# Optimization experiments

Hardware: AMD Instinct MI355X
Metric: run time of the kernel (lower is better)

Reference implementation:

```python
import jax, jax.numpy as jnp
import numpy as np

H = 768
NH = 12
HD = H // NH
NDIM = 5
LN_EPS = 1e-5


def setup_inputs() -> dict:
    key = jax.random.key(0)
    ks = jax.random.split(key, 12)
    B, S = 4, 2048
    xavier = lambda k: jax.random.uniform(k, (H, H), jnp.float32, -1.0, 1.0) * np.sqrt(6.0 / (H + H))
    return {
        "hidden_states": jax.random.normal(ks[0], (B, S, H), jnp.float32),
        "Wq": xavier(ks[1]), "bq": jnp.zeros((H,), jnp.float32),
        "Wk": xavier(ks[2]), "bk": jnp.zeros((H,), jnp.float32),
        "Wv": xavier(ks[3]), "bv": jnp.zeros((H,), jnp.float32),
        "Wo": xavier(ks[4]), "bo": jnp.zeros((H,), jnp.float32),
        # per-dimension, per-head scalar biases (torch init: zeros; use small randn so grads are non-trivial)
        "dim_biases": 0.02 * jax.random.normal(ks[5], (NDIM, NH), jnp.float32),
        "ln_gamma": jnp.ones((H,), jnp.float32),
        "ln_beta": jnp.zeros((H,), jnp.float32),
        "attention_mask": jax.random.randint(ks[6], (4, 2048), 0, 2, jnp.int32),
        "dimension_idx": 2,
    }


def reference(hidden_states, Wq, bq, Wk, bk, Wv, bv, Wo, bo, dim_biases,
              ln_gamma, ln_beta, attention_mask, dimension_idx):
    B, S, _ = hidden_states.shape
    residual = hidden_states
    # torch nn.Linear: x @ W.T + b
    q = (hidden_states @ Wq.T + bq).reshape(B, S, NH, HD).transpose(0, 2, 1, 3)  # [B,NH,S,HD]
    k = (hidden_states @ Wk.T + bk).reshape(B, S, NH, HD).transpose(0, 2, 1, 3)
    v = (hidden_states @ Wv.T + bv).reshape(B, S, NH, HD).transpose(0, 2, 1, 3)

    scores = jnp.einsum("bhqd,bhkd->bhqk", q, k) / np.sqrt(HD)  # [B,NH,S,S]
    if dimension_idx is not None and dimension_idx < NDIM:
        scores = scores + dim_biases[dimension_idx][None, :, None, None]
    # mask over key positions, broadcast over heads and queries
    scores = jnp.where(attention_mask[:, None, None, :] == 0, -jnp.inf, scores)
    attn = jax.nn.softmax(scores, axis=-1)

    ctx = jnp.einsum("bhqk,bhkd->bhqd", attn, v)  # [B,NH,S,HD]
    ctx = ctx.transpose(0, 2, 1, 3).reshape(B, S, H)
    out = ctx @ Wo.T + bo

    y = out + residual
    mu = jnp.mean(y, axis=-1, keepdims=True)
    var = jnp.var(y, axis=-1, keepdims=True)
    y = (y - mu) / jnp.sqrt(var + LN_EPS) * ln_gamma + ln_beta
    return y
```

## Files before the change

### kernel.cpp

```cpp
#include <hip/hip_runtime.h>
#include <hip/hip_bf16.h>

#define HH    768
#define NHEAD 12
#define HDIM  64
#define BB    4
#define SS    2048
#define MM    (BB*SS)
#define NDIMS 5
#define WEL   (HH*HH)
#define LOG2E 1.44269504088896f
#define QSCALE 0.180336881f

typedef unsigned short u16;
typedef __attribute__((ext_vector_type(8))) short short8;
typedef __attribute__((ext_vector_type(4))) short short4v;
typedef __attribute__((ext_vector_type(4))) float floatx4;
typedef __attribute__((ext_vector_type(16))) float floatx16;
typedef __attribute__((ext_vector_type(4))) unsigned int uint4v;
typedef __attribute__((ext_vector_type(2))) unsigned int uint2v;

__device__ __forceinline__ float bf2f(u16 u) {
    return __uint_as_float(((unsigned int)u) << 16);
}
__device__ __forceinline__ u16 f2bf(float f) {
    unsigned int x = __float_as_uint(f);
    unsigned int r = (x + 0x7fffu + ((x >> 16) & 1u)) >> 16;
    return (u16)r;
}
__device__ __forceinline__ unsigned int pack_bf16x2(float a, float b) {
    float2 f2 = make_float2(a, b);
    __hip_bfloat162 h2 = __float22bfloat162_rn(f2);
    return *reinterpret_cast<unsigned int*>(&h2);
}
__device__ __forceinline__ void gld16(const u16* g, u16* l) {
    __builtin_amdgcn_global_load_lds(
        (const __attribute__((address_space(1))) unsigned int*)g,
        (__attribute__((address_space(3))) unsigned int*)l, 16, 0, 0);
}

__global__ __launch_bounds__(256) void f32_to_bf16(
    const float* __restrict__ in, u16* __restrict__ out, int n8)
{
    int i = blockIdx.x * 256 + threadIdx.x;
    if (i >= n8) return;
    float4 a = ((const float4*)in)[i*2];
    float4 b = ((const float4*)in)[i*2 + 1];
    ushort4 lo, hi;
    lo.x = f2bf(a.x); lo.y = f2bf(a.y); lo.z = f2bf(a.z); lo.w = f2bf(a.w);
    hi.x = f2bf(b.x); hi.y = f2bf(b.y); hi.z = f2bf(b.z); hi.w = f2bf(b.w);
    ((ushort4*)out)[i*2]     = lo;
    ((ushort4*)out)[i*2 + 1] = hi;
}

#define XCVT_BLKS ((MM*HH)/8/256)
#define WCVT_BLKS (WEL/8/256)
__global__ __launch_bounds__(256) void cvt_all(
    const float* __restrict__ x,
    const float* __restrict__ W0, const float* __restrict__ W1,
    const float* __restrict__ W2, const float* __restrict__ W3,
    u16* __restrict__ xb, u16* __restrict__ wb)
{
    const int bid = blockIdx.x;
    const float* src;
    u16* dst;
    int i;
    if (bid < XCVT_BLKS) {
        src = x; dst = xb; i = bid * 256 + threadIdx.x;
    } else {
        const int wsel = (bid - XCVT_BLKS) / WCVT_BLKS;
        src = (wsel == 0) ? W0 : (wsel == 1) ? W1 : (wsel == 2) ? W2 : W3;
        dst = wb + (size_t)wsel * WEL;
        i = ((bid - XCVT_BLKS) % WCVT_BLKS) * 256 + threadIdx.x;
    }
    float4 a = ((const float4*)src)[i*2];
    float4 b = ((const float4*)src)[i*2 + 1];
    ushort4 lo, hi;
    lo.x = f2bf(a.x); lo.y = f2bf(a.y); lo.z = f2bf(a.z); lo.w = f2bf(a.w);
    hi.x = f2bf(b.x); hi.y = f2bf(b.y); hi.z = f2bf(b.z); hi.w = f2bf(b.w);
    ((ushort4*)dst)[i*2]     = lo;
    ((ushort4*)dst)[i*2 + 1] = hi;
}

__device__ __forceinline__ void gemm_gld_body(
    const u16* __restrict__ Xb, const u16* __restrict__ Wrows,
    const float* __restrict__ biasL, u16* __restrict__ outL, int i0)
{
    __shared__ u16 Xs[128][64];
    __shared__ u16 Ws[128][64];
    const int t = threadIdx.x;
    const int w = t >> 6, lane = t & 63;
    const int wy = w >> 1, wx = w & 1;
    const int m = lane & 31, hh = lane >> 5;

    const int grow = lane >> 3;
    const int cg   = (lane & 7) ^ grow;

    floatx16 acc[2][2];
    #pragma unroll
    for (int am = 0; am < 2; ++am)
        #pragma unroll
        for (int bn = 0; bn < 2; ++bn)
            #pragma unroll
            for (int r = 0; r < 16; ++r) acc[am][bn][r] = 0.f;

    for (int k0 = 0; k0 < HH; k0 += 64) {
        __syncthreads();
        #pragma unroll
        for (int j = 0; j < 4; ++j) {
            const int r = w*32 + j*8;
            gld16(Xb    + (size_t)(i0 + r + grow)*HH + k0 + cg*8, &Xs[r][0]);
            gld16(Wrows + (size_t)(r + grow)*HH      + k0 + cg*8, &Ws[r][0]);
        }
        __syncthreads();

        #pragma unroll
        for (int kh = 0; kh < 4; ++kh) {
            const int ch = kh*2 + hh;
            short8 af[2], bf[2];
            #pragma unroll
            for (int am = 0; am < 2; ++am) {
                const int row = wy*64 + am*32 + m;
                af[am] = *(const short8*)&Xs[row][(ch ^ (m & 7))*8];
            }
            #pragma unroll
            for (int bn = 0; bn < 2; ++bn) {
                const int row = wx*64 + bn*32 + m;
                bf[bn] = *(const short8*)&Ws[row][(ch ^ (m & 7))*8];
            }
            #pragma unroll
            for (int am = 0; am < 2; ++am)
                #pragma unroll
                for (int bn = 0; bn < 2; ++bn)
                    acc[am][bn] = __builtin_amdgcn_mfma_f32_32x32x16_bf16(
                        af[am], bf[bn], acc[am][bn], 0, 0, 0);
        }
    }

    float bb[2];
    #pragma unroll
    for (int bn = 0; bn < 2; ++bn) bb[bn] = biasL[wx*64 + bn*32 + m];
    #pragma unroll
    for (int am = 0; am < 2; ++am)
        #pragma unroll
        for (int bn = 0; bn < 2; ++bn)
            #pragma unroll
            for (int r = 0; r < 16; ++r) {
                int row = i0 + wy*64 + am*32 + (r & 3) + 8*(r >> 2) + 4*hh;
                outL[(size_t)row*HH + wx*64 + bn*32 + m] = f2bf(acc[am][bn][r] + bb[bn]);
            }
}

__global__ __launch_bounds__(256) void gemm_gld_qkv(
    const u16* __restrict__ Xb, const u16* __restrict__ Wb3,
    const float* __restrict__ bq, const float* __restrict__ bk, const float* __restrict__ bv,
    u16* __restrict__ oq, u16* __restrict__ ok, u16* __restrict__ ov)
{
    const int j0 = blockIdx.x * 128;
    const int sel = j0 / HH;
    const int lj = j0 - sel * HH;
    const float* bias = (sel == 0) ? bq : (sel == 1) ? bk : bv;
    u16* out = (sel == 0) ? oq : (sel == 1) ? ok : ov;
    gemm_gld_body(Xb, Wb3 + (size_t)j0 * HH, bias + lj, out + lj, blockIdx.y * 128);
}

__global__ __launch_bounds__(256) void gemm_gld_single(
    const u16* __restrict__ Xb, const u16* __restrict__ Wb,
    const float* __restrict__ bias, u16* __restrict__ out)
{
    const int j0 = blockIdx.x * 128;
    gemm_gld_body(Xb, Wb + (size_t)j0 * HH, bias + j0, out + j0, blockIdx.y * 128);
}

__global__ __launch_bounds__(256) void gemm_mfma_nt(
    const u16* __restrict__ Xb, const float* __restrict__ W,
    const float* __restrict__ bias, u16* __restrict__ out)
{
    __shared__ u16 Xs[128][40];
    __shared__ u16 Wt[64][40];
    const int t = threadIdx.x;
    const int w = t >> 6, lane = t & 63;
    const int c = lane & 15, qd = lane >> 4;
    const int i0 = blockIdx.y * 128, j0 = blockIdx.x * 64;
    const int xrow = t >> 1, xoff = (t & 1) * 16;
    const int wn = t >> 2, woff = (t & 3) * 8;

    floatx4 acc[2][4];
    #pragma unroll
    for (int mt = 0; mt < 2; ++mt)
        #pragma unroll
        for (int nt = 0; nt < 4; ++nt) acc[mt][nt] = (floatx4){0.f,0.f,0.f,0.f};

    for (int k0 = 0; k0 < HH; k0 += 32) {
        uint4 xa  = *(const uint4*)(Xb + (size_t)(i0 + xrow)*HH + k0 + xoff);
        uint4 xb2 = *(const uint4*)(Xb + (size_t)(i0 + xrow)*HH + k0 + xoff + 8);
        float4 wa = *(const float4*)(W + (size_t)(j0 + wn)*HH + k0 + woff);
        float4 wb = *(const float4*)(W + (size_t)(j0 + wn)*HH + k0 + woff + 4);
        __syncthreads();
        *(uint4*)&Xs[xrow][xoff]     = xa;
        *(uint4*)&Xs[xrow][xoff + 8] = xb2;
        ushort4 w0, w1;
        w0.x = f2bf(wa.x); w0.y = f2bf(wa.y); w0.z = f2bf(wa.z); w0.w = f2bf(wa.w);
        w1.x = f2bf(wb.x); w1.y = f2bf(wb.y); w1.z = f2bf(wb.z); w1.w = f2bf(wb.w);
        *(ushort4*)&Wt[wn][woff]     = w0;
        *(ushort4*)&Wt[wn][woff + 4] = w1;
        __syncthreads();

        short8 a0 = *(const short8*)&Xs[w*32 + c][qd*8];
        short8 a1 = *(const short8*)&Xs[w*32 + 16 + c][qd*8];
        #pragma unroll
        for (int nt = 0; nt < 4; ++nt) {
            short8 bfr = *(const short8*)&Wt[nt*16 + c][qd*8];
            acc[0][nt] = __builtin_amdgcn_mfma_f32_16x16x32_bf16(a0, bfr, acc[0][nt], 0, 0, 0);
            acc[1][nt] = __builtin_amdgcn_mfma_f32_16x16x32_bf16(a1, bfr, acc[1][nt], 0, 0, 0);
        }
    }

    float bv[4];
    #pragma unroll
    for (int nt = 0; nt < 4; ++nt) bv[nt] = bias[j0 + nt*16 + c];
    #pragma unroll
    for (int mt = 0; mt < 2; ++mt)
        #pragma unroll
        for (int nt = 0; nt < 4; ++nt)
            #pragma unroll
            for (int r = 0; r < 4; ++r)
                out[(size_t)(i0 + w*32 + mt*16 + qd*4 + r)*HH + j0 + nt*16 + c] =
                    f2bf(acc[mt][nt][r] + bv[nt]);
}

__global__ __launch_bounds__(256, 3) void attn_mfma32(
    const u16* __restrict__ Q, const u16* __restrict__ K, const u16* __restrict__ V,
    const float* __restrict__ dim_biases, const int* __restrict__ mask,
    const int* __restrict__ dim_idx_p, u16* __restrict__ ctx)
{
    __shared__ u16 Ks[2][64][64];
    __shared__ u16 Vt[2][64][68];
    __shared__ float madd[2][64];

    const int t = threadIdx.x;
    const int w = t >> 6, lane = t & 63;
    const int ql = lane & 31, hi = lane >> 5;
    const int sw7 = ql & 7;

    const int flat = blockIdx.x + 16 * (blockIdx.y + 12 * blockIdx.z);
    const int swz  = (flat & 7) * 96 + (flat >> 3);
    const int q0 = (swz & 15) * 128;
    const int h  = (swz >> 4) % NHEAD;
    const int b  = swz / (16 * NHEAD);

    const int didx = *dim_idx_p;
    const float db2 = ((didx < NDIMS) ? dim_biases[didx*NHEAD + h] : 0.f) * LOG2E;

    const int grow = lane >> 3;
    const int cg   = (lane & 7) ^ grow;
    const int vkp = t & 31;
    const int vdg = (t >> 5) * 8;

    short8 ones;
    #pragma unroll
    for (int j = 0; j < 8; ++j) ones[j] = (short)0x3F80;

    short8 qv[4];
    {
        const u16* qsrc = Q + ((size_t)(b*SS + q0 + w*32 + ql))*HH + h*HDIM + 8*hi;
        #pragma unroll
        for (int s = 0; s < 4; ++s) {
            ushort4 u0 = *(const ushort4*)(qsrc + s*16);
            ushort4 u1 = *(const ushort4*)(qsrc + s*16 + 4);
            const u16 uu[8] = {u0.x,u0.y,u0.z,u0.w,u1.x,u1.y,u1.z,u1.w};
            #pragma unroll
            for (int j = 0; j < 8; ++j)
                qv[s][j] = (short)f2bf(bf2f(uu[j]) * QSCALE);
        }
    }

    floatx16 o[2], lacc;
    #pragma unroll
    for (int r = 0; r < 16; ++r) { o[0][r] = 0.f; o[1][r] = 0.f; lacc[r] = 0.f; }

    uint4 VA, VB;
    int mreg = 0;

    auto issueK = [&](int kt, int buf) {
        #pragma unroll
        for (int j = 0; j < 2; ++j) {
            const int rbase = w*16 + j*8;
            gld16(K + (size_t)(b*SS + kt*64 + rbase + grow)*HH + h*HDIM + cg*8,
                  &Ks[buf][rbase][0]);
        }
    };
    auto issueV = [&](int kt) {
        const u16* va = V + ((size_t)(b*SS + kt*64 + 2*vkp))*HH + h*HDIM + vdg;
        VA = *(const uint4*)va;
        VB = *(const uint4*)(va + HH);
        if (t < 64) mreg = mask[(size_t)b*SS + kt*64 + t];
    };
    auto writeV = [&](int buf) {
        const unsigned* Aw = (const unsigned*)&VA;
        const unsigned* Bw = (const unsigned*)&VB;
        #pragma unroll
        for (int i2 = 0; i2 < 4; ++i2) {
            unsigned a = Aw[i2], bb = Bw[i2];
            *(unsigned*)&Vt[buf][vdg + 2*i2][2*vkp]     = (a & 0xffffu) | (bb << 16);
            *(unsigned*)&Vt[buf][vdg + 2*i2 + 1][2*vkp] = (a >> 16) | (bb & 0xffff0000u);
        }
        if (t < 64) madd[buf][t] = (mreg != 0) ? db2 : -1e30f;
    };

    issueK(0, 0);
    issueV(0);
    writeV(0);

    for (int kt = 0; kt < SS/64; ++kt) {
        const int cur = kt & 1;
        __syncthreads();
        const bool more = (kt + 1 < SS/64);
        if (more) { issueK(kt + 1, cur ^ 1); issueV(kt + 1); }

        #pragma unroll
        for (int kblk = 0; kblk < 2; ++kblk) {
            const u16* kb = &Ks[cur][kblk*32 + ql][0];

            floatx16 z;
            #pragma unroll
            for (int qq = 0; qq < 4; ++qq) {
                float4 mv = *(const float4*)&madd[cur][kblk*32 + qq*8 + 4*hi];
                z[qq*4+0] = mv.x; z[qq*4+1] = mv.y; z[qq*4+2] = mv.z; z[qq*4+3] = mv.w;
            }
            short8 kf[4];
            #pragma unroll
            for (int s = 0; s < 4; ++s)
                kf[s] = *(const short8*)(kb + ((s*2 + hi) ^ sw7)*8);
            __builtin_amdgcn_s_setprio(1);
            #pragma unroll
            for (int s = 0; s < 4; ++s)
                z = __builtin_amdgcn_mfma_f32_32x32x16_bf16(kf[s], qv[s], z, 0, 0, 0);
            __builtin_amdgcn_s_setprio(0);

            #pragma unroll
            for (int r = 0; r < 16; ++r) z[r] = __builtin_amdgcn_exp2f(z[r]);

            #pragma unroll
            for (int ks = 0; ks < 2; ++ks) {
                unsigned x0 = pack_bf16x2(z[ks*8 + 0], z[ks*8 + 1]);
                unsigned y0 = pack_bf16x2(z[ks*8 + 4], z[ks*8 + 5]);
                unsigned x1 = pack_bf16x2(z[ks*8 + 2], z[ks*8 + 3]);
                unsigned y1 = pack_bf16x2(z[ks*8 + 6], z[ks*8 + 7]);
                uint2v s0 = __builtin_amdgcn_permlane32_swap(x0, y0, false, false);
                uint2v s1 = __builtin_amdgcn_permlane32_swap(x1, y1, false, false);
                uint4v pv; pv[0] = s0[0]; pv[1] = s1[0]; pv[2] = s0[1]; pv[3] = s1[1];
                short8 pa = __builtin_bit_cast(short8, pv);

                const int ck = kblk*4 + ks*2 + hi;
                const u16* vp0 = &Vt[cur][ql][ck*8];
                const u16* vp1 = &Vt[cur][32 + ql][ck*8];
                short4v a0 = *(const short4v*)vp0;
                short4v a1 = *(const short4v*)(vp0 + 4);
                short4v b0 = *(const short4v*)vp1;
                short4v b1 = *(const short4v*)(vp1 + 4);
                short8 vf0, vf1;
                #pragma unroll
                for (int j = 0; j < 4; ++j) {
                    vf0[j] = a0[j]; vf0[4+j] = a1[j];
                    vf1[j] = b0[j]; vf1[4+j] = b1[j];
                }

                __builtin_amdgcn_s_setprio(1);
                lacc = __builtin_amdgcn_mfma_f32_32x32x16_bf16(pa, ones, lacc, 0, 0, 0);
                o[0] = __builtin_amdgcn_mfma_f32_32x32x16_bf16(pa, vf0, o[0], 0, 0, 0);
                o[1] = __builtin_amdgcn_mfma_f32_32x32x16_bf16(pa, vf1, o[1], 0, 0, 0);
                __builtin_amdgcn_s_setprio(0);
            }
        }

        if (more) writeV(cur ^ 1);
    }

    #pragma unroll
    for (int r = 0; r < 16; ++r) {
        float l = lacc[r];
        float inv = (l > 0.f) ? 1.f / l : 0.f;
        const int qrow = q0 + w*32 + (r & 3) + 8*(r >> 2) + 4*hi;
        u16* dst = ctx + ((size_t)(b*SS + qrow))*HH + h*HDIM + ql;
        dst[0]  = f2bf(o[0][r] * inv);
        dst[32] = f2bf(o[1][r] * inv);
    }
}

__global__ __launch_bounds__(256) void add_ln_wave(
    const u16* __restrict__ proj, const float* __restrict__ resid,
    const float* __restrict__ gamma, const float* __restrict__ beta,
    float* __restrict__ out)
{
    const int t = threadIdx.x, w = t >> 6, lane = t & 63;
    const int row = blockIdx.x * 4 + w;
    const size_t base = (size_t)row * HH + lane * 12;
    const int gbase = lane * 12;

    float x[12];
    #pragma unroll
    for (int j = 0; j < 3; ++j) {
        ushort4 p = *(const ushort4*)(proj + base + j*4);
        float4  r = *(const float4*)(resid + base + j*4);
        x[j*4+0] = bf2f(p.x) + r.x;
        x[j*4+1] = bf2f(p.y) + r.y;
        x[j*4+2] = bf2f(p.z) + r.z;
        x[j*4+3] = bf2f(p.w) + r.w;
    }
    float s = 0.f, ss = 0.f;
    #pragma unroll
    for (int j = 0; j < 12; ++j) { s += x[j]; ss += x[j]*x[j]; }
    #pragma unroll
    for (int off = 1; off < 64; off <<= 1) {
        s  += __shfl_xor(s, off);
        ss += __shfl_xor(ss, off);
    }
    float mean = s * (1.f/768.f);
    float var  = ss * (1.f/768.f) - mean*mean;
    float rstd = rsqrtf(fmaxf(var, 0.f) + 1e-5f);
    #pragma unroll
    for (int j = 0; j < 3; ++j) {
        float4 g = *(const float4*)(gamma + gbase + j*4);
        float4 bt = *(const float4*)(beta + gbase + j*4);
        float4 y;
        y.x = (x[j*4+0]-mean)*rstd*g.x + bt.x;
        y.y = (x[j*4+1]-mean)*rstd*g.y + bt.y;
        y.z = (x[j*4+2]-mean)*rstd*g.z + bt.z;
        y.w = (x[j*4+3]-mean)*rstd*g.w + bt.w;
        *(float4*)(out + base + j*4) = y;
    }
}

extern "C" void kernel_launch(void* const* d_in, const int* in_sizes, int n_in,
                              void* d_out, int out_size, void* d_ws, size_t ws_size,
                              hipStream_t stream)
{
    (void)in_sizes; (void)n_in; (void)out_size;
    const float* x    = (const float*)d_in[0];
    const float* Wq   = (const float*)d_in[1];
    const float* bq   = (const float*)d_in[2];
    const float* Wk   = (const float*)d_in[3];
    const float* bk   = (const float*)d_in[4];
    const float* Wv   = (const float*)d_in[5];
    const float* bv   = (const float*)d_in[6];
    const float* Wo   = (const float*)d_in[7];
    const float* bo   = (const float*)d_in[8];
    const float* dimb = (const float*)d_in[9];
    const float* gam  = (const float*)d_in[10];
    const float* bet  = (const float*)d_in[11];
    const int* mask   = (const int*)d_in[12];
    const int* didx   = (const int*)d_in[13];

    const size_t N = (size_t)MM * HH;
    if (ws_size < 4 * N * sizeof(u16)) return;
    u16* ws = (u16*)d_ws;
    u16* q    = ws;
    u16* kbuf = ws + N;
    u16* vbuf = ws + 2*N;
    u16* slot3 = ws + 3*N;
    u16* xb   = slot3;
    u16* ctx  = slot3;
    u16* proj = q;

    const bool bigws = ws_size >= (4 * N + 4 * (size_t)WEL) * sizeof(u16);
    u16* wb = ws + 4 * N;

    if (bigws) {
        cvt_all<<<XCVT_BLKS + 4*WCVT_BLKS, 256, 0, stream>>>(x, Wq, Wk, Wv, Wo, xb, wb);
        gemm_gld_qkv<<<dim3(3*HH/128, MM/128), 256, 0, stream>>>(
            xb, wb, bq, bk, bv, q, kbuf, vbuf);
    } else {
        f32_to_bf16<<<(int)(N/8/256), 256, 0, stream>>>(x, xb, (int)(N/8));
        dim3 gg(HH/64, MM/128);
        gemm_mfma_nt<<<gg, 256, 0, stream>>>(xb, Wq, bq, q);
        gemm_mfma_nt<<<gg, 256, 0, stream>>>(xb, Wk, bk, kbuf);
        gemm_mfma_nt<<<gg, 256, 0, stream>>>(xb, Wv, bv, vbuf);
    }
    attn_mfma32<<<dim3(SS/128, NHEAD, BB), 256, 0, stream>>>(q, kbuf, vbuf, dimb, mask, didx, ctx);
    if (bigws) gemm_gld_single<<<dim3(HH/128, MM/128), 256, 0, stream>>>(ctx, wb + 3*WEL, bo, proj);
    else {
        dim3 gg(HH/64, MM/128);
        gemm_mfma_nt<<<gg, 256, 0, stream>>>(ctx, Wo, bo, proj);
    }
    add_ln_wave<<<MM/4, 256, 0, stream>>>(proj, x, gam, bet, (float*)d_out);
}
```

Before: 245.6 us.

## Swizzle QKV GEMM block order and add 64-row tile kernel for output projection

The QKV GEMM now remaps its flat block index so that groups of 8 consecutive blocks are spread across the grid, aiming for better L2/cache locality or XCD distribution. The output projection switches from 128x128 tiles to a new 64x128 tile kernel with the same swizzled block mapping, doubling the block count to 768 for better CU occupancy on the 256-CU part. Smaller tiles reduce data reuse per block and add a new kernel body to maintain.

```diff
diff --git a/kernel.cpp b/kernel.cpp
--- a/kernel.cpp
+++ b/kernel.cpp
@@ -156,20 +156,74 @@
     const float* __restrict__ bq, const float* __restrict__ bk, const float* __restrict__ bv,
     u16* __restrict__ oq, u16* __restrict__ ok, u16* __restrict__ ov)
 {
-    const int j0 = blockIdx.x * 128;
+    const int flat = blockIdx.x + 18 * blockIdx.y;
+    const int swz  = (flat & 7) * 144 + (flat >> 3);
+    const int j0 = (swz % 18) * 128;
+    const int i0 = (swz / 18) * 128;
     const int sel = j0 / HH;
     const int lj = j0 - sel * HH;
     const float* bias = (sel == 0) ? bq : (sel == 1) ? bk : bv;
     u16* out = (sel == 0) ? oq : (sel == 1) ? ok : ov;
-    gemm_gld_body(Xb, Wb3 + (size_t)j0 * HH, bias + lj, out + lj, blockIdx.y * 128);
-}
-
-__global__ __launch_bounds__(256) void gemm_gld_single(
+    gemm_gld_body(Xb, Wb3 + (size_t)j0 * HH, bias + lj, out + lj, i0);
+}
+
+__global__ __launch_bounds__(256) void gemm_gld_m64(
     const u16* __restrict__ Xb, const u16* __restrict__ Wb,
     const float* __restrict__ bias, u16* __restrict__ out)
 {
-    const int j0 = blockIdx.x * 128;
-    gemm_gld_body(Xb, Wb + (size_t)j0 * HH, bias + j0, out + j0, blockIdx.y * 128);
+    __shared__ u16 Xs[64][64];
+    __shared__ u16 Ws[128][64];
+    const int t = threadIdx.x;
+    const int w = t >> 6, lane = t & 63;
+    const int m = lane & 31, hh = lane >> 5;
+    const int grow = lane >> 3;
+    const int cg   = (lane & 7) ^ grow;
+
+    const int flat = blockIdx.x + 6 * blockIdx.y;
+    const int swz  = (flat & 7) * 96 + (flat >> 3);
+    const int j0 = (swz % 6) * 128;
+    const int i0 = (swz / 6) * 64;
+
+    floatx16 acc[2];
+    #pragma unroll
+    for (int am = 0; am < 2; ++am)
+        #pragma unroll
+        for (int r = 0; r < 16; ++r) acc[am][r] = 0.f;
+
+    for (int k0 = 0; k0 < HH; k0 += 64) {
+        __syncthreads();
+        #pragma unroll
+        for (int j = 0; j < 2; ++j) {
+            const int r = w*16 + j*8;
+            gld16(Xb + (size_t)(i0 + r + grow)*HH + k0 + cg*8, &Xs[r][0]);
+        }
+        #pragma unroll
+        for (int j = 0; j < 4; ++j) {
+            const int r = w*32 + j*8;
+            gld16(Wb + (size_t)(j0 + r + grow)*HH + k0 + cg*8, &Ws[r][0]);
+        }
+        __syncthreads();
+
+        #pragma unroll
+        for (int kh = 0; kh < 4; ++kh) {
+            const int ch = kh*2 + hh;
+            short8 af[2], bf;
+            af[0] = *(const short8*)&Xs[m][(ch ^ (m & 7))*8];
+            af[1] = *(const short8*)&Xs[32 + m][(ch ^ (m & 7))*8];
+            bf    = *(const short8*)&Ws[w*32 + m][(ch ^ (m & 7))*8];
+            acc[0] = __builtin_amdgcn_mfma_f32_32x32x16_bf16(af[0], bf, acc[0], 0, 0, 0);
+            acc[1] = __builtin_amdgcn_mfma_f32_32x32x16_bf16(af[1], bf, acc[1], 0, 0, 0);
+        }
+    }
+
+    const float bb = bias[j0 + w*32 + m];
+    #pragma unroll
+    for (int am = 0; am < 2; ++am)
+        #pragma unroll
+        for (int r = 0; r < 16; ++r) {
+            int row = i0 + am*32 + (r & 3) + 8*(r >> 2) + 4*hh;
+            out[(size_t)row*HH + j0 + w*32 + m] = f2bf(acc[am][r] + bb);
+        }
 }
 
 __global__ __launch_bounds__(256) void gemm_mfma_nt(
@@ -478,7 +532,7 @@
         gemm_mfma_nt<<<gg, 256, 0, stream>>>(xb, Wv, bv, vbuf);
     }
     attn_mfma32<<<dim3(SS/128, NHEAD, BB), 256, 0, stream>>>(q, kbuf, vbuf, dimb, mask, didx, ctx);
-    if (bigws) gemm_gld_single<<<dim3(HH/128, MM/128), 256, 0, stream>>>(ctx, wb + 3*WEL, bo, proj);
+    if (bigws) gemm_gld_m64<<<dim3(HH/128, MM/64), 256, 0, stream>>>(ctx, wb + 3*WEL, bo, proj);
     else {
         dim3 gg(HH/64, MM/128);
         gemm_mfma_nt<<<gg, 256, 0, stream>>>(ctx, Wo, bo, proj);
```

After: 245.8 us. No clear change (+0.1%).
